# Performance work log

Measured on AMD Instinct MI355X. Metric: run time of the kernel, lower is better.

The kernel has to match this reference:

```python
import jax, jax.numpy as jnp
import numpy as np

B, S, E, H, DH = 256, 256, 384, 6, 64
NEG_INF = -1e9


def setup_inputs() -> dict:
    key = jax.random.key(0)
    ks = jax.random.split(key, 8)
    sc = 0.02
    return {
        "x": jax.random.normal(ks[0], (B, S, E), jnp.float32),
        "Wq": jax.random.normal(ks[1], (H, E, DH), jnp.float32) * sc,
        "Wk": jax.random.normal(ks[2], (H, E, DH), jnp.float32) * sc,
        "Wv": jax.random.normal(ks[3], (H, E, DH), jnp.float32) * sc,
        "Wp": jax.random.normal(ks[4], (E, E), jnp.float32) * sc,
        "bp": jnp.zeros((E,), jnp.float32),
        "W1": jax.random.normal(ks[5], (E, 4 * E), jnp.float32) * sc,
        "b1": jnp.zeros((4 * E,), jnp.float32),
        "W2": jax.random.normal(ks[6], (4 * E, E), jnp.float32) * sc,
        "b2": jnp.zeros((E,), jnp.float32),
        "g1": jnp.ones((E,), jnp.float32),
        "be1": jnp.zeros((E,), jnp.float32),
        "g2": jnp.ones((E,), jnp.float32),
        "be2": jnp.zeros((E,), jnp.float32),
    }


def _layernorm(x, g, b, eps=1e-5):
    mu = jnp.mean(x, axis=-1, keepdims=True)
    var = jnp.mean(jnp.square(x - mu), axis=-1, keepdims=True)
    return (x - mu) * jax.lax.rsqrt(var + eps) * g + b


def reference(x, Wq, Wk, Wv, Wp, bp, W1, b1, W2, b2, g1, be1, g2, be2):
    # --- pre-attention LayerNorm ---
    h = _layernorm(x, g1, be1)
    # --- multi-head causal self-attention (all heads vectorized) ---
    q = jnp.einsum('bse,hed->bhsd', h, Wq)
    k = jnp.einsum('bse,hed->bhsd', h, Wk)
    v = jnp.einsum('bse,hed->bhsd', h, Wv)
    scores = jnp.einsum('bhsd,bhtd->bhst', q, k) * (DH ** -0.5)
    causal = jnp.tril(jnp.ones((S, S), dtype=bool))
    scores = jnp.where(causal, scores, NEG_INF)
    att = jax.nn.softmax(scores, axis=-1)  # dropout = identity at eval
    o = jnp.einsum('bhst,bhtd->bhsd', att, v)
    o = o.transpose(0, 2, 1, 3).reshape(x.shape[0], S, E)  # concat heads
    x = x + (o @ Wp + bp)
    # --- FFN block ---
    h2 = _layernorm(x, g2, be2)
    ffn = jax.nn.relu(h2 @ W1 + b1) @ W2 + b2
    return x + ffn
```

## Files before the change

kernel.cpp:

```cpp
#include <hip/hip_runtime.h>
#include <hip/hip_bf16.h>
#include <stdint.h>

typedef __bf16 bf16_t;
typedef __bf16 bf16x2 __attribute__((ext_vector_type(2)));
typedef __bf16 bf16x8 __attribute__((ext_vector_type(8)));
typedef float f32x4 __attribute__((ext_vector_type(4)));

#define NB 256
#define NS 256
#define NE 384
#define NH 6
#define ND 64
#define NM (NB*NS)

__device__ __forceinline__ f32x4 mfma16(bf16x8 a, bf16x8 b, f32x4 c) {
    return __builtin_amdgcn_mfma_f32_16x16x32_bf16(a, b, c, 0, 0, 0);
}

__device__ __forceinline__ void cp16_async(const bf16_t* g, const bf16_t* l) {
    __builtin_amdgcn_global_load_lds(
        (__attribute__((address_space(1))) void*)g,
        (__attribute__((address_space(3))) void*)l, 16, 0, 0);
}

__global__ void wqkv_trans(const float* __restrict__ Wq, const float* __restrict__ Wk,
                           const float* __restrict__ Wv, bf16_t* __restrict__ Wcat)
{
    int i = blockIdx.x * 256 + threadIdx.x;
    if (i >= NH*NE*ND) return;
    int d = i & 63;
    int e = (i >> 6) % NE;
    int h = i / (NE*ND);
    int n = h*64 + d;
    Wcat[(size_t)n*NE + e]         = (bf16_t)Wq[i];
    Wcat[(size_t)(384 + n)*NE + e] = (bf16_t)Wk[i];
    Wcat[(size_t)(768 + n)*NE + e] = (bf16_t)Wv[i];
}

__global__ void wtrans(const float* __restrict__ src, bf16_t* __restrict__ dst, int K, int N)
{
    int i = blockIdx.x * 256 + threadIdx.x;
    if (i >= K*N) return;
    int k = i / N, n = i % N;
    dst[(size_t)n*K + k] = (bf16_t)src[i];
}

__global__ __launch_bounds__(256) void ln_kernel(
    const float* __restrict__ x, const float* __restrict__ g,
    const float* __restrict__ be, bf16_t* __restrict__ o)
{
    const int wave = threadIdx.x >> 6, lane = threadIdx.x & 63;
    const int row = blockIdx.x * 4 + wave;
    const float* xr = x + (size_t)row * NE;
    float v[6]; float s = 0.f, sq = 0.f;
    #pragma unroll
    for (int i = 0; i < 6; i++) { v[i] = xr[i*64 + lane]; s += v[i]; sq += v[i]*v[i]; }
    #pragma unroll
    for (int off = 32; off > 0; off >>= 1) { s += __shfl_xor(s, off); sq += __shfl_xor(sq, off); }
    const float mean = s * (1.f/NE);
    const float rstd = rsqrtf(sq * (1.f/NE) - mean*mean + 1e-5f);
    bf16_t* orow = o + (size_t)row * NE;
    #pragma unroll
    for (int i = 0; i < 6; i++) {
        int e = i*64 + lane;
        orow[e] = (bf16_t)((v[i] - mean) * rstd * g[e] + be[e]);
    }
}

template<int OUT_MODE, bool RELU>
__global__ __launch_bounds__(512, 1) void gemm_areg(
    const bf16_t* __restrict__ A, int lda,
    const bf16_t* __restrict__ Bt, int ldb,
    void* __restrict__ outp, const float* __restrict__ bias,
    const float* __restrict__ res, int N)
{
    __shared__ bf16_t sW[3][24576];
    const int tid = threadIdx.x;
    const int wv = tid >> 6, lane = tid & 63;
    const int l15 = lane & 15, quad = lane >> 4;
    const int m0 = blockIdx.x * 128;
    const int nc = N >> 6;

    uint32_t bo[6];
    #pragma unroll
    for (int i = 0; i < 6; i++) {
        int idx = i*512 + tid;
        int row = idx / 48, sp = idx % 48;
        bo[i] = (uint32_t)(row * (ldb*2)) + (((uint32_t)(sp*16)) ^ ((uint32_t)((row & 7) << 4)));
    }
    const char* Bbase = (const char*)Bt;

    auto issue = [&](int c, int slot) {
        const char* src = Bbase + (size_t)c * ((size_t)64 * ldb * 2);
        bf16_t* dstb = (bf16_t*)((char*)&sW[slot][0] + tid*16);
        #pragma unroll
        for (int i = 0; i < 6; i++)
            cp16_async((const bf16_t*)(src + bo[i]), dstb + i*4096);
    };

    const int arow = m0 + wv*16 + l15;
    bf16x8 a[12];
    #pragma unroll
    for (int kc = 0; kc < 12; kc++)
        a[kc] = *(const bf16x8*)(A + (size_t)arow*lda + kc*32 + quad*8);

    issue(0, 0);
    issue(1, 1);

    const int swz = (l15 & 7) << 4;
    int cb = 0, ns = 2;
    for (int j = 0; j < nc; ++j) {
        asm volatile("s_barrier" ::: "memory");
        if (j + 2 < nc) issue(j + 2, ns);
        asm volatile("s_waitcnt vmcnt(12)\n\ts_barrier" ::: "memory");

        #pragma unroll
        for (int ni = 0; ni < 4; ni++) {
            f32x4 acc = {0.f, 0.f, 0.f, 0.f};
            const int rowoff = (ni*16 + l15) * 768;
            #pragma unroll
            for (int kc = 0; kc < 12; kc++) {
                const int kb = (kc*64 + quad*16) ^ swz;
                bf16x8 wf = *(const bf16x8*)((const char*)&sW[cb][0] + rowoff + kb);
                acc = mfma16(a[kc], wf, acc);
            }
            const int gn = j*64 + ni*16 + l15;
            const float bv = bias ? bias[gn] : 0.f;
            #pragma unroll
            for (int rr = 0; rr < 4; rr++) {
                const int gm = m0 + wv*16 + quad*4 + rr;
                float v = acc[rr] + bv;
                if (res)  v += res[(size_t)gm*N + gn];
                if (RELU) v = fmaxf(v, 0.f);
                if (OUT_MODE == 1) {
                    int sel = (gn >= 768) ? 2 : ((gn >= 384) ? 1 : 0);
                    int within = gn - sel*384;
                    int b = gm >> 8, s2 = gm & 255, h = within >> 6, d = within & 63;
                    ((bf16_t*)outp)[(size_t)sel*((size_t)NM*384) +
                                    (((size_t)b*NH + h)*NS + s2)*ND + d] = (bf16_t)v;
                } else if (OUT_MODE == 2) {
                    ((float*)outp)[(size_t)gm*N + gn] = v;
                } else {
                    ((bf16_t*)outp)[(size_t)gm*N + gn] = (bf16_t)v;
                }
            }
        }
        cb = (cb == 2) ? 0 : cb + 1;
        ns = (ns == 2) ? 0 : ns + 1;
    }
}

__global__ __launch_bounds__(512, 1) void gemm_ffn2(
    const bf16_t* __restrict__ hid,
    const bf16_t* __restrict__ W2t,
    float* __restrict__ outp,
    const float* __restrict__ b2)
{
    __shared__ bf16_t sW[3][24576];
    const int tid = threadIdx.x;
    const int wv = tid >> 6, lane = tid & 63;
    const int l15 = lane & 15, quad = lane >> 4;
    const int m0 = blockIdx.x * 128;

    uint32_t bo[6];
    #pragma unroll
    for (int i = 0; i < 6; i++) {
        int idx = i*512 + tid;
        int row = idx >> 3, sp = idx & 7;
        bo[i] = (uint32_t)(row * 3072) + (((uint32_t)(sp*16)) ^ ((uint32_t)((row & 7) << 4)));
    }

    auto issue = [&](int c, int slot) {
        const char* src = (const char*)W2t + c*128;
        bf16_t* dstb = (bf16_t*)((char*)&sW[slot][0] + tid*16);
        #pragma unroll
        for (int i = 0; i < 6; i++)
            cp16_async((const bf16_t*)(src + bo[i]), dstb + i*4096);
    };

    const bf16_t* Ap = hid + (size_t)(m0 + wv*16 + l15)*1536 + quad*8;

    f32x4 acc[24];
    #pragma unroll
    for (int i = 0; i < 24; i++) acc[i] = (f32x4){0.f, 0.f, 0.f, 0.f};

    issue(0, 0);
    issue(1, 1);

    bf16x8 aC0 = *(const bf16x8*)(Ap);
    bf16x8 aC1 = *(const bf16x8*)(Ap + 32);
    bf16x8 aN0, aN1;

    const int swz = (l15 & 7) << 4;
    int cb = 0, ns = 2;
    for (int j = 0; j < 24; ++j) {
        asm volatile("s_barrier" ::: "memory");
        if (j + 2 < 24) issue(j + 2, ns);
        asm volatile("s_waitcnt vmcnt(12)\n\ts_barrier" ::: "memory");
        if (j + 1 < 24) {
            aN0 = *(const bf16x8*)(Ap + (j+1)*64);
            aN1 = *(const bf16x8*)(Ap + (j+1)*64 + 32);
        }
        #pragma unroll
        for (int ni = 0; ni < 24; ni++) {
            const int rowoff = (ni*16 + l15) * 128;
            bf16x8 w0 = *(const bf16x8*)((const char*)&sW[cb][0] + rowoff + ((quad*16) ^ swz));
            bf16x8 w1 = *(const bf16x8*)((const char*)&sW[cb][0] + rowoff + ((64 + quad*16) ^ swz));
            acc[ni] = mfma16(aC0, w0, acc[ni]);
            acc[ni] = mfma16(aC1, w1, acc[ni]);
        }
        aC0 = aN0; aC1 = aN1;
        cb = (cb == 2) ? 0 : cb + 1;
        ns = (ns == 2) ? 0 : ns + 1;
    }

    #pragma unroll
    for (int ni = 0; ni < 24; ni++) {
        const int gn = ni*16 + l15;
        const float bv = b2[gn];
        #pragma unroll
        for (int rr = 0; rr < 4; rr++) {
            const int gm = m0 + wv*16 + quad*4 + rr;
            float* p = outp + (size_t)gm*384 + gn;
            *p = *p + acc[ni][rr] + bv;
        }
    }
}

__global__ __launch_bounds__(256) void attn_kernel(
    const bf16_t* __restrict__ Qg, const bf16_t* __restrict__ Kg,
    const bf16_t* __restrict__ Vg, bf16_t* __restrict__ Og)
{
    __shared__ bf16_t sK[256*72];
    __shared__ bf16_t sVT[64*264];
    __shared__ bf16_t sQ[64*72];
    __shared__ bf16_t sS[64*264];
    __shared__ float sMax[64*4];
    __shared__ float sSum[64*4];
    __shared__ float sRowSum[64];

    const int tid = threadIdx.x;
    const int wave = tid >> 6, lane = tid & 63;
    const int l15 = lane & 15, quad = lane >> 4;
    const int bh = blockIdx.x;
    const int b = bh / NH, h = bh % NH;
    const size_t base = (size_t)bh * (NS*ND);
    const bf16_t* Qb = Qg + base;
    const bf16_t* Kb = Kg + base;
    const bf16_t* Vb = Vg + base;

    #pragma unroll
    for (int it = 0; it < 8; it++) {
        int idx = it*256 + tid;
        int t = idx >> 3, c = idx & 7;
        bf16x8 kv = *(const bf16x8*)(Kb + t*64 + c*8);
        *(bf16x8*)&sK[t*72 + c*8] = kv;
        bf16x8 vv = *(const bf16x8*)(Vb + t*64 + c*8);
        #pragma unroll
        for (int j = 0; j < 8; j++) sVT[(c*8 + j)*264 + t] = vv[j];
    }

    const int r = lane;
    const int p = wave;
    const f32x4 zero = {0.f, 0.f, 0.f, 0.f};

    for (int mt = 0; mt < 4; mt++) {
        __syncthreads();
        #pragma unroll
        for (int it = 0; it < 2; it++) {
            int idx = it*256 + tid;
            int qr = idx >> 3, c = idx & 7;
            *(bf16x8*)&sQ[qr*72 + c*8] = *(const bf16x8*)(Qb + (64*mt + qr)*64 + c*8);
        }
        __syncthreads();
        if (wave <= mt) {
            const int ct = wave;
            bf16x8 bk[2][4];
            #pragma unroll
            for (int ks = 0; ks < 2; ks++)
                #pragma unroll
                for (int ni = 0; ni < 4; ni++)
                    bk[ks][ni] = *(const bf16x8*)&sK[(64*ct + 16*ni + l15)*72 + ks*32 + quad*8];
            #pragma unroll
            for (int mi = 0; mi < 4; mi++) {
                bf16x8 a0 = *(const bf16x8*)&sQ[(16*mi + l15)*72 + quad*8];
                bf16x8 a1 = *(const bf16x8*)&sQ[(16*mi + l15)*72 + 32 + quad*8];
                f32x4 sc[4];
                #pragma unroll
                for (int ni = 0; ni < 4; ni++) sc[ni] = zero;
                #pragma unroll
                for (int ni = 0; ni < 4; ni++) sc[ni] = mfma16(a0, bk[0][ni], sc[ni]);
                #pragma unroll
                for (int ni = 0; ni < 4; ni++) sc[ni] = mfma16(a1, bk[1][ni], sc[ni]);
                #pragma unroll
                for (int ni = 0; ni < 4; ni++)
                    #pragma unroll
                    for (int rr = 0; rr < 4; rr++)
                        sS[(16*mi + quad*4 + rr)*264 + 64*ct + 16*ni + l15] =
                            (bf16_t)(sc[ni][rr] * 0.125f);
            }
        }
        __syncthreads();
        const int sg = 64*mt + r;
        float mx = -INFINITY;
        if (p <= mt) {
            #pragma unroll
            for (int c = 0; c < 8; c++) {
                bf16x8 v8 = *(const bf16x8*)&sS[r*264 + 64*p + c*8];
                #pragma unroll
                for (int j = 0; j < 8; j++) {
                    int t = 64*p + c*8 + j;
                    float v = (float)v8[j];
                    mx = (t <= sg) ? fmaxf(mx, v) : mx;
                }
            }
        }
        sMax[r*4 + p] = mx;
        __syncthreads();
        const float rmax = fmaxf(fmaxf(sMax[r*4+0], sMax[r*4+1]),
                                 fmaxf(sMax[r*4+2], sMax[r*4+3]));
        float sum = 0.f;
        if (p <= mt) {
            #pragma unroll
            for (int c = 0; c < 8; c++) {
                bf16x8 v8 = *(const bf16x8*)&sS[r*264 + 64*p + c*8];
                bf16x8 e8;
                #pragma unroll
                for (int j = 0; j < 8; j++) {
                    int t = 64*p + c*8 + j;
                    float e = 0.f;
                    if (t <= sg) e = __expf((float)v8[j] - rmax);
                    sum += e;
                    e8[j] = (bf16_t)e;
                }
                *(bf16x8*)&sS[r*264 + 64*p + c*8] = e8;
            }
        }
        sSum[r*4 + p] = sum;
        __syncthreads();
        if (p == 0) sRowSum[r] = sSum[r*4+0] + sSum[r*4+1] + sSum[r*4+2] + sSum[r*4+3];
        __syncthreads();
        f32x4 oacc[4];
        #pragma unroll
        for (int ni = 0; ni < 4; ni++) oacc[ni] = zero;
        for (int kt = 0; kt <= mt; kt++) {
            bf16x8 a = *(const bf16x8*)&sS[(16*p + l15)*264 + 64*kt + quad*8];
            #pragma unroll
            for (int ni = 0; ni < 4; ni++) {
                bf16x8 bv = *(const bf16x8*)&sVT[(16*ni + l15)*264 + 64*kt + quad*8];
                oacc[ni] = mfma16(a, bv, oacc[ni]);
            }
        }
        #pragma unroll
        for (int ni = 0; ni < 4; ni++) {
            #pragma unroll
            for (int rr = 0; rr < 4; rr++) {
                int lrow = 16*p + quad*4 + rr;
                float inv = 1.0f / sRowSum[lrow];
                int srow_g = 64*mt + lrow;
                int d = 16*ni + l15;
                Og[((size_t)(b*NS + srow_g))*NE + h*ND + d] = (bf16_t)(oacc[ni][rr] * inv);
            }
        }
    }
}

extern "C" void kernel_launch(void* const* d_in, const int* in_sizes, int n_in,
                              void* d_out, int out_size, void* d_ws, size_t ws_size,
                              hipStream_t stream)
{
    (void)in_sizes; (void)n_in; (void)out_size; (void)ws_size;
    const float* x   = (const float*)d_in[0];
    const float* Wq  = (const float*)d_in[1];
    const float* Wk  = (const float*)d_in[2];
    const float* Wv  = (const float*)d_in[3];
    const float* Wp  = (const float*)d_in[4];
    const float* bp  = (const float*)d_in[5];
    const float* W1  = (const float*)d_in[6];
    const float* b1  = (const float*)d_in[7];
    const float* W2  = (const float*)d_in[8];
    const float* b2  = (const float*)d_in[9];
    const float* g1  = (const float*)d_in[10];
    const float* be1 = (const float*)d_in[11];
    const float* g2  = (const float*)d_in[12];
    const float* be2 = (const float*)d_in[13];
    float* out = (float*)d_out;

    char* ws = (char*)d_ws;
    const size_t SZ = (size_t)NM * NE * 2;
    bf16_t* h_bf  = (bf16_t*)(ws);
    bf16_t* q_bf  = (bf16_t*)(ws + SZ);
    bf16_t* k_bf  = (bf16_t*)(ws + 2*SZ);
    bf16_t* v_bf  = (bf16_t*)(ws + 3*SZ);
    bf16_t* o_bf  = (bf16_t*)(ws);
    bf16_t* h2_bf = (bf16_t*)(ws);
    bf16_t* hid   = (bf16_t*)(ws + SZ);
    char* wb = ws + 4*SZ;
    bf16_t* Wcat = (bf16_t*)(wb);
    bf16_t* Wpt  = (bf16_t*)(wb + 884736);
    bf16_t* W1t  = (bf16_t*)(wb + 884736 + 294912);
    bf16_t* W2t  = (bf16_t*)(wb + 884736 + 294912 + 1179648);

    wqkv_trans<<<(NH*NE*ND + 255)/256, 256, 0, stream>>>(Wq, Wk, Wv, Wcat);
    wtrans<<<(NE*NE + 255)/256, 256, 0, stream>>>(Wp, Wpt, NE, NE);
    wtrans<<<(NE*4*NE + 255)/256, 256, 0, stream>>>(W1, W1t, NE, 4*NE);
    wtrans<<<(NE*4*NE + 255)/256, 256, 0, stream>>>(W2, W2t, 4*NE, NE);

    ln_kernel<<<NM/4, 256, 0, stream>>>(x, g1, be1, h_bf);

    gemm_areg<1,false><<<NM/128, 512, 0, stream>>>(
        h_bf, NE, Wcat, NE, q_bf, nullptr, nullptr, 1152);

    attn_kernel<<<NB*NH, 256, 0, stream>>>(q_bf, k_bf, v_bf, o_bf);

    gemm_areg<2,false><<<NM/128, 512, 0, stream>>>(
        o_bf, NE, Wpt, NE, out, bp, x, NE);

    ln_kernel<<<NM/4, 256, 0, stream>>>(out, g2, be2, h2_bf);

    for (int half = 0; half < 2; half++) {
        const size_t roff = (size_t)half * 32768;
        const bf16_t* h2h = h2_bf + roff * NE;
        float* outh = out + roff * NE;
        gemm_areg<3,true><<<32768/128, 512, 0, stream>>>(
            h2h, NE, W1t, NE, hid, b1, nullptr, 1536);
        gemm_ffn2<<<32768/128, 512, 0, stream>>>(hid, W2t, outh, b2);
    }
}
```

Baseline: 878.1 us.

## Drop K/Q shared staging in attention, load fragments from global, raise occupancy

The attention kernel no longer stages K and Q in LDS. Each wave reads its Q rows and the K fragments straight from global memory and computes scores by query-row tile instead of by key tile. This cuts LDS use so two blocks can fit per CU (launch_bounds 256,2), and it balances score work across waves. It also caches score rows in registers between the max and exp passes, skips the causal mask test on full tiles, and raises wave priority around the MFMA sections. In exchange, K fragments are read redundantly from global/L2 by every wave, and register pressure goes up.

```diff
diff --git a/kernel.cpp b/kernel.cpp
--- a/kernel.cpp
+++ b/kernel.cpp
@@ -228,13 +228,11 @@
     }
 }
 
-__global__ __launch_bounds__(256) void attn_kernel(
+__global__ __launch_bounds__(256, 2) void attn_kernel(
     const bf16_t* __restrict__ Qg, const bf16_t* __restrict__ Kg,
     const bf16_t* __restrict__ Vg, bf16_t* __restrict__ Og)
 {
-    __shared__ bf16_t sK[256*72];
     __shared__ bf16_t sVT[64*264];
-    __shared__ bf16_t sQ[64*72];
     __shared__ bf16_t sS[64*264];
     __shared__ float sMax[64*4];
     __shared__ float sSum[64*4];
@@ -254,8 +252,6 @@
     for (int it = 0; it < 8; it++) {
         int idx = it*256 + tid;
         int t = idx >> 3, c = idx & 7;
-        bf16x8 kv = *(const bf16x8*)(Kb + t*64 + c*8);
-        *(bf16x8*)&sK[t*72 + c*8] = kv;
         bf16x8 vv = *(const bf16x8*)(Vb + t*64 + c*8);
         #pragma unroll
         for (int j = 0; j < 8; j++) sVT[(c*8 + j)*264 + t] = vv[j];
@@ -267,52 +263,51 @@
 
     for (int mt = 0; mt < 4; mt++) {
         __syncthreads();
-        #pragma unroll
-        for (int it = 0; it < 2; it++) {
-            int idx = it*256 + tid;
-            int qr = idx >> 3, c = idx & 7;
-            *(bf16x8*)&sQ[qr*72 + c*8] = *(const bf16x8*)(Qb + (64*mt + qr)*64 + c*8);
-        }
-        __syncthreads();
-        if (wave <= mt) {
-            const int ct = wave;
-            bf16x8 bk[2][4];
-            #pragma unroll
-            for (int ks = 0; ks < 2; ks++)
-                #pragma unroll
-                for (int ni = 0; ni < 4; ni++)
-                    bk[ks][ni] = *(const bf16x8*)&sK[(64*ct + 16*ni + l15)*72 + ks*32 + quad*8];
-            #pragma unroll
-            for (int mi = 0; mi < 4; mi++) {
-                bf16x8 a0 = *(const bf16x8*)&sQ[(16*mi + l15)*72 + quad*8];
-                bf16x8 a1 = *(const bf16x8*)&sQ[(16*mi + l15)*72 + 32 + quad*8];
+
+        {
+            const int qrow = 64*mt + 16*wave + l15;
+            bf16x8 a0 = *(const bf16x8*)(Qb + (size_t)qrow*64 + quad*8);
+            bf16x8 a1 = *(const bf16x8*)(Qb + (size_t)qrow*64 + 32 + quad*8);
+            for (int ct = 0; ct <= mt; ct++) {
                 f32x4 sc[4];
                 #pragma unroll
                 for (int ni = 0; ni < 4; ni++) sc[ni] = zero;
+                __builtin_amdgcn_s_setprio(1);
                 #pragma unroll
-                for (int ni = 0; ni < 4; ni++) sc[ni] = mfma16(a0, bk[0][ni], sc[ni]);
-                #pragma unroll
-                for (int ni = 0; ni < 4; ni++) sc[ni] = mfma16(a1, bk[1][ni], sc[ni]);
+                for (int ni = 0; ni < 4; ni++) {
+                    const bf16_t* kr = Kb + (size_t)(64*ct + 16*ni + l15)*64;
+                    bf16x8 b0 = *(const bf16x8*)(kr + quad*8);
+                    bf16x8 b1 = *(const bf16x8*)(kr + 32 + quad*8);
+                    sc[ni] = mfma16(a0, b0, sc[ni]);
+                    sc[ni] = mfma16(a1, b1, sc[ni]);
+                }
+                __builtin_amdgcn_s_setprio(0);
                 #pragma unroll
                 for (int ni = 0; ni < 4; ni++)
                     #pragma unroll
                     for (int rr = 0; rr < 4; rr++)
-                        sS[(16*mi + quad*4 + rr)*264 + 64*ct + 16*ni + l15] =
+                        sS[(16*wave + quad*4 + rr)*264 + 64*ct + 16*ni + l15] =
                             (bf16_t)(sc[ni][rr] * 0.125f);
             }
         }
         __syncthreads();
+
         const int sg = 64*mt + r;
+        const bool active = (p <= mt);
+        const bool full = (p < mt);
         float mx = -INFINITY;
-        if (p <= mt) {
+        bf16x8 v8r[8];
+        if (active) {
+            #pragma unroll
+            for (int c = 0; c < 8; c++)
+                v8r[c] = *(const bf16x8*)&sS[r*264 + 64*p + c*8];
             #pragma unroll
             for (int c = 0; c < 8; c++) {
-                bf16x8 v8 = *(const bf16x8*)&sS[r*264 + 64*p + c*8];
                 #pragma unroll
                 for (int j = 0; j < 8; j++) {
                     int t = 64*p + c*8 + j;
-                    float v = (float)v8[j];
-                    mx = (t <= sg) ? fmaxf(mx, v) : mx;
+                    float v = (float)v8r[c][j];
+                    mx = (full || t <= sg) ? fmaxf(mx, v) : mx;
                 }
             }
         }
@@ -321,16 +316,15 @@
         const float rmax = fmaxf(fmaxf(sMax[r*4+0], sMax[r*4+1]),
                                  fmaxf(sMax[r*4+2], sMax[r*4+3]));
         float sum = 0.f;
-        if (p <= mt) {
+        if (active) {
             #pragma unroll
             for (int c = 0; c < 8; c++) {
-                bf16x8 v8 = *(const bf16x8*)&sS[r*264 + 64*p + c*8];
                 bf16x8 e8;
                 #pragma unroll
                 for (int j = 0; j < 8; j++) {
                     int t = 64*p + c*8 + j;
                     float e = 0.f;
-                    if (t <= sg) e = __expf((float)v8[j] - rmax);
+                    if (full || t <= sg) e = __expf((float)v8r[c][j] - rmax);
                     sum += e;
                     e8[j] = (bf16_t)e;
                 }
@@ -341,16 +335,19 @@
         __syncthreads();
         if (p == 0) sRowSum[r] = sSum[r*4+0] + sSum[r*4+1] + sSum[r*4+2] + sSum[r*4+3];
         __syncthreads();
+
         f32x4 oacc[4];
         #pragma unroll
         for (int ni = 0; ni < 4; ni++) oacc[ni] = zero;
         for (int kt = 0; kt <= mt; kt++) {
             bf16x8 a = *(const bf16x8*)&sS[(16*p + l15)*264 + 64*kt + quad*8];
+            __builtin_amdgcn_s_setprio(1);
             #pragma unroll
             for (int ni = 0; ni < 4; ni++) {
                 bf16x8 bv = *(const bf16x8*)&sVT[(16*ni + l15)*264 + 64*kt + quad*8];
                 oacc[ni] = mfma16(a, bv, oacc[ni]);
             }
+            __builtin_amdgcn_s_setprio(0);
         }
         #pragma unroll
         for (int ni = 0; ni < 4; ni++) {
```

Result: faster. 860.5 us (-2.0%).
